# Kernel optimization log

Hardware: AMD Instinct MI355X
Metric: run time of the kernel (lower is better)

## Reference

```python
import jax, jax.numpy as jnp
import numpy as np

B, C, H, W = 32, 1, 28, 896
WW = WS = 28
S = (W - WW) // WS + 1  # 32 windows
CONV_DIM, FC_DIM, NUM_CLASSES = 64, 128, 83
FC_IN = CONV_DIM * (H // 2) * (WW // 2)  # 64*14*14 = 12544


def setup_inputs() -> dict:
    key = jax.random.key(0)
    ks = jax.random.split(key, 9)
    sc = 0.05
    return {
        "x": jax.random.normal(ks[0], (B, C, H, W), jnp.float32),
        "conv1_w": jax.random.normal(ks[1], (CONV_DIM, C, 3, 3), jnp.float32) * sc,
        "conv1_b": jax.random.normal(ks[2], (CONV_DIM,), jnp.float32) * sc,
        "conv2_w": jax.random.normal(ks[3], (CONV_DIM, CONV_DIM, 3, 3), jnp.float32) * sc,
        "conv2_b": jax.random.normal(ks[4], (CONV_DIM,), jnp.float32) * sc,
        "fc1_w": jax.random.normal(ks[5], (FC_DIM, FC_IN), jnp.float32) * sc,
        "fc1_b": jax.random.normal(ks[6], (FC_DIM,), jnp.float32) * sc,
        "fc2_w": jax.random.normal(ks[7], (NUM_CLASSES, FC_DIM), jnp.float32) * sc,
        "fc2_b": jax.random.normal(ks[8], (NUM_CLASSES,), jnp.float32) * sc,
    }


def _conv_relu(x, w, b):
    # 3x3 conv, stride 1, padding 1 (torch Conv2d padding=1), then ReLU
    y = jax.lax.conv_general_dilated(
        x, w, window_strides=(1, 1), padding=((1, 1), (1, 1)),
        dimension_numbers=("NCHW", "OIHW", "NCHW"))
    return jax.nn.relu(y + b[None, :, None, None])


def reference(x, conv1_w, conv1_b, conv2_w, conv2_b, fc1_w, fc1_b, fc2_w, fc2_b):
    Bx = x.shape[0]
    # WS == WW -> non-overlapping windows; extract all S windows at once via reshape
    # (B, C, H, S*WW) -> (B*S, C, H, WW)
    win = x.reshape(Bx, C, H, S, WW).transpose(0, 3, 1, 2, 4).reshape(Bx * S, C, H, WW)
    h = _conv_relu(win, conv1_w, conv1_b)
    h = _conv_relu(h, conv2_w, conv2_b)
    # MaxPool2d(2)
    h = jax.lax.reduce_window(h, -jnp.inf, jax.lax.max,
                              window_dimensions=(1, 1, 2, 2),
                              window_strides=(1, 1, 2, 2), padding="VALID")
    # dropout is identity in eval mode
    h = h.reshape(Bx * S, FC_IN)  # torch.flatten(x, 1) on NCHW matches row-major reshape
    h = jax.nn.relu(h @ fc1_w.T + fc1_b)
    logits = h @ fc2_w.T + fc2_b  # (B*S, num_classes)
    # -> (B, num_classes, S) as in the torch module
    return logits.reshape(Bx, S, NUM_CLASSES).transpose(0, 2, 1)
```

## Files before the change

### kernel.cpp

```cpp
#include <hip/hip_runtime.h>
#include <hip/hip_bf16.h>


typedef __attribute__((ext_vector_type(8))) short short8;
typedef __attribute__((ext_vector_type(4))) float f32x4;

#define WB1_E   0u
#define WB2_E   2048u
#define WFC1_E  38912u
#define WFC2_E  1644544u
#define POOL_E  1656832u
#define PART_B  29003776u

__device__ __forceinline__ unsigned short f2bf(float f) {
  unsigned u = __float_as_uint(f);
  u += 0x7fffu + ((u >> 16) & 1u);
  return (unsigned short)(u >> 16);
}

__global__ __launch_bounds__(256) void prep_kernel(
    const float* __restrict__ w1, const float* __restrict__ c1b,
    const float* __restrict__ w2, const float* __restrict__ wfc1,
    const float* __restrict__ wfc2, unsigned short* __restrict__ ws16)
{
  int i = blockIdx.x * blockDim.x + threadIdx.x;
  if (i < 2048) {
    int j = i & 7, l = (i >> 3) & 63, nt = i >> 9;
    int n = nt * 16 + (l & 15), k = 8 * (l >> 4) + j;
    float v = (k < 9) ? w1[n * 9 + k] : (k == 9 ? c1b[n] : 0.f);
    ws16[WB1_E + i] = f2bf(v);
  } else if (i < 38912) {
    int i2 = i - 2048;
    int j = i2 & 7, l = (i2 >> 3) & 63, rest = i2 >> 9;
    int ks = rest % 18, nt = rest / 18;
    int n = nt * 16 + (l & 15);
    int kk = ks * 32 + 8 * (l >> 4) + j;
    int dydx = kk >> 6, ci = kk & 63;
    ws16[WB2_E + i2] = f2bf(w2[n * 576 + ci * 9 + dydx]);
  } else if (i < 1644544) {
    int i2 = i - 38912;
    int j = i2 & 7, l = (i2 >> 3) & 63, rest = i2 >> 9;
    int ks = rest % 392, nt = rest / 392;
    int fcn = nt * 16 + (l & 15);
    int kp = ks * 32 + 8 * (l >> 4) + j;
    int co = kp & 63, r2 = kp >> 6;
    int oxp = r2 % 14, oyp = r2 / 14;
    ws16[WFC1_E + i2] = f2bf(wfc1[fcn * 12544 + co * 196 + oyp * 14 + oxp]);
  } else if (i < 1656832) {
    int i2 = i - 1644544;
    int j = i2 & 7, l = (i2 >> 3) & 63, rest = i2 >> 9;
    int ks = rest & 3, nt = rest >> 2;
    int cls = nt * 16 + (l & 15);
    int k = ks * 32 + 8 * (l >> 4) + j;
    float v = (cls < 83) ? wfc2[cls * 128 + k] : 0.f;
    ws16[WFC2_E + i2] = f2bf(v);
  }
}

__global__ __launch_bounds__(512, 4) void conv_kernel(
    const float* __restrict__ x, const float* __restrict__ c2b,
    unsigned short* __restrict__ ws16)
{
  extern __shared__ char smem[];
  unsigned short* xw = (unsigned short*)(smem + 69120);

  const int tid = threadIdx.x;
  const int wave = tid >> 6, lane = tid & 63;
  const int g = lane >> 4, l15 = lane & 15;
  const int bid = blockIdx.x;
  const int n = bid >> 1, hf = bid & 1;
  const int r0 = hf ? 16 : 0;
  const int rlo = hf ? 15 : 0;
  const int M1 = hf ? 364 : 476;
  const int T1 = hf ? 23 : 30;
  const int T2 = hf ? 21 : 28;

  const short8* wb1 = (const short8*)(ws16 + WB1_E);
  const short8* wb2 = (const short8*)(ws16 + WB2_E);
  unsigned short* poolg = ws16 + POOL_E + (unsigned)n * 12544u;

  short8 z8 = {0, 0, 0, 0, 0, 0, 0, 0};
  short8* l8 = (short8*)smem;
  for (int idx = tid; idx < 4320; idx += 512) l8[idx] = z8;
  {
    const float* xg = x + (n >> 5) * 25088 + (n & 31) * 28;
    for (int i = tid; i < 784; i += 512)
      xw[i] = f2bf(xg[(i / 28) * 896 + (i % 28)]);
  }
  __syncthreads();

  {
    short8 b1f[4];
#pragma unroll
    for (int nt = 0; nt < 4; ++nt) b1f[nt] = wb1[nt * 64 + lane];
    for (int mt = wave; mt < T1; mt += 8) {
      int m = mt * 16 + l15;
      bool mval = m < M1;
      int mc = mval ? m : M1 - 1;
      int rr = rlo + mc / 28, ox = mc % 28;
      short8 a;
#pragma unroll
      for (int j = 0; j < 8; ++j) {
        int k = 8 * g + j;
        int dy = (k >= 6) ? 2 : ((k >= 3) ? 1 : 0);
        int dx = k - 3 * dy;
        int iy = rr + dy - 1, ix = ox + dx - 1;
        bool valid = (k < 9) && mval && iy >= 0 && iy < 28 && ix >= 0 && ix < 28;
        int idx = valid ? iy * 28 + ix : 0;
        unsigned short v = xw[idx];
        short r = valid ? (short)v : (short)0;
        a[j] = (k == 9) ? (short)0x3F80 : r;
      }
      f32x4 d[4];
#pragma unroll
      for (int nt = 0; nt < 4; ++nt) {
        f32x4 zz = {0.f, 0.f, 0.f, 0.f};
        d[nt] = __builtin_amdgcn_mfma_f32_16x16x32_bf16(b1f[nt], a, zz, 0, 0, 0);
      }
      if (mval) {
        int lr = rr - r0 + 1;
        int sp = lr * 30 + ox + 1;
        unsigned base = (unsigned)sp * 128u;
        unsigned swz = ((unsigned)sp & 7u) << 4;
#pragma unroll
        for (int nt = 0; nt < 4; ++nt)
#pragma unroll
          for (int t = 0; t < 2; ++t) {
            int co2 = nt * 16 + 4 * g + 2 * t;
            unsigned pk = (unsigned)f2bf(fmaxf(d[nt][2 * t], 0.f)) |
                          ((unsigned)f2bf(fmaxf(d[nt][2 * t + 1], 0.f)) << 16);
            *(unsigned*)(smem + (base + (((unsigned)(co2 * 2)) ^ swz))) = pk;
          }
      }
    }
  }
  __syncthreads();

  {
    const int ntp = (wave < 4) ? 0 : 2;
    const int mg = wave & 3;
    float c2bv[2];
#pragma unroll
    for (int tn = 0; tn < 2; ++tn) c2bv[tn] = c2b[(ntp + tn) * 16 + l15];
    const int w4 = l15 >> 2;
    const int oyw = 2 * (w4 >> 1) + ((l15 >> 1) & 1);
    const int oxw = 2 * (w4 & 1) + (l15 & 1);
    int spb[7];
#pragma unroll
    for (int mi = 0; mi < 7; ++mi) {
      int mt = mg + 4 * mi;
      int ryy = (mt * 37) >> 8;
      int rx = mt - 7 * ryy;
      spb[mi] = (4 * ryy + oyw) * 30 + 4 * rx + oxw;
    }
    f32x4 acc[7][2];
#pragma unroll
    for (int mi = 0; mi < 7; ++mi) {
      f32x4 zz = {0.f, 0.f, 0.f, 0.f};
      acc[mi][0] = zz; acc[mi][1] = zz;
    }
#pragma unroll 1
    for (int phase = 0; phase < 6; ++phase) {
      short8 bfr[2][3];
#pragma unroll
      for (int tn = 0; tn < 2; ++tn)
#pragma unroll
        for (int ks = 0; ks < 3; ++ks)
          bfr[tn][ks] = wb2[((ntp + tn) * 18 + phase * 3 + ks) * 64 + lane];
      int dspv[3], cixv[3];
#pragma unroll
      for (int ks = 0; ks < 3; ++ks) {
        int ksg = phase * 3 + ks;
        int dydx = ksg >> 1;
        int dy = (dydx * 11) >> 5;
        int dx = dydx - 3 * dy;
        dspv[ks] = dy * 30 + dx;
        cixv[ks] = ((ksg & 1) << 6) + 16 * g;
      }
#pragma unroll
      for (int mi = 0; mi < 7; ++mi) {
        int mt = mg + 4 * mi;
        if (mt < T2) {
#pragma unroll
          for (int ks = 0; ks < 3; ++ks) {
            int sp = spb[mi] + dspv[ks];
            unsigned off = (unsigned)sp * 128u +
                           (((unsigned)cixv[ks]) ^ ((((unsigned)sp) & 7u) << 4));
            short8 a = *(const short8*)(smem + off);
            acc[mi][0] = __builtin_amdgcn_mfma_f32_16x16x32_bf16(a, bfr[0][ks], acc[mi][0], 0, 0, 0);
            acc[mi][1] = __builtin_amdgcn_mfma_f32_16x16x32_bf16(a, bfr[1][ks], acc[mi][1], 0, 0, 0);
          }
        }
      }
    }
    const int yb = hf ? 8 : 0;
#pragma unroll
    for (int mi = 0; mi < 7; ++mi) {
      int mt = mg + 4 * mi;
      if (mt < T2) {
        int ryy = (mt * 37) >> 8;
        int rx = mt - 7 * ryy;
        int oyp = yb + 2 * ryy + (g >> 1);
        int oxp = 2 * rx + (g & 1);
#pragma unroll
        for (int tn = 0; tn < 2; ++tn) {
          int co = (ntp + tn) * 16 + l15;
          f32x4 v = acc[mi][tn];
          float p = fmaxf(fmaxf(v[0], v[1]), fmaxf(v[2], v[3]));
          p = fmaxf(p + c2bv[tn], 0.f);
          poolg[(oyp * 14 + oxp) * 64 + co] = f2bf(p);
        }
      }
    }
  }
}

__global__ __launch_bounds__(512) void fc1_kernel(unsigned short* __restrict__ ws16)
{
  extern __shared__ char smem[];
  short8* A8 = (short8*)smem;
  const int tid = threadIdx.x;
  const int wave = tid >> 6, lane = tid & 63;
  const int g = lane >> 4, l15 = lane & 15;
  const int ig = blockIdx.x >> 2, q = blockIdx.x & 3;
  const short8* pool8 = (const short8*)(ws16 + POOL_E);
  const short8* wf1 = (const short8*)(ws16 + WFC1_E);
  {
    int img = tid >> 5, l32 = tid & 31;
    const short8* src = pool8 + (ig * 16 + img) * 1568 + q * 392;
#pragma unroll
    for (int j = 0; j < 13; ++j) {
      int idx = l32 + 32 * j;
      if (idx < 392) A8[img * 393 + idx] = src[idx];
    }
  }
  __syncthreads();
  f32x4 acc = {0.f, 0.f, 0.f, 0.f};
  const short8* wbase = wf1 + (wave * 392 + q * 98) * 64 + lane;
#pragma unroll 2
  for (int ks = 0; ks < 98; ++ks) {
    short8 b = wbase[ks * 64];
    short8 a = A8[l15 * 393 + ks * 4 + g];
    acc = __builtin_amdgcn_mfma_f32_16x16x32_bf16(a, b, acc, 0, 0, 0);
  }
  _Float16* part = (_Float16*)((char*)ws16 + PART_B);
  int base = ((q * 64 + ig) * 16 + 4 * g) * 128 + wave * 16 + l15;
#pragma unroll
  for (int i = 0; i < 4; ++i) part[base + i * 128] = (_Float16)acc[i];
}

__global__ __launch_bounds__(512) void fc2_kernel(
    const float* __restrict__ b1, const float* __restrict__ b2,
    const unsigned short* __restrict__ ws16, float* __restrict__ out)
{
  __shared__ unsigned short h_s[16 * 136];
  const int tid = threadIdx.x;
  const int wave = tid >> 6, lane = tid & 63;
  const int g = lane >> 4, l15 = lane & 15;
  const int ig = blockIdx.x;
  const _Float16* part = (const _Float16*)((const char*)ws16 + PART_B);
#pragma unroll
  for (int t = 0; t < 4; ++t) {
    int u = tid + 512 * t;
    int img = u >> 7, fcn = u & 127;
    float s = 0.f;
#pragma unroll
    for (int q2 = 0; q2 < 4; ++q2)
      s += (float)part[((q2 * 64 + ig) * 16 + img) * 128 + fcn];
    h_s[img * 136 + fcn] = f2bf(fmaxf(s + b1[fcn], 0.f));
  }
  __syncthreads();
  if (wave < 6) {
    const short8* wf2 = (const short8*)(ws16 + WFC2_E);
    const short8* h8 = (const short8*)h_s;
    f32x4 a2 = {0.f, 0.f, 0.f, 0.f};
#pragma unroll
    for (int ks = 0; ks < 4; ++ks) {
      short8 b = wf2[(wave * 4 + ks) * 64 + lane];
      short8 a = h8[l15 * 17 + ks * 4 + g];
      a2 = __builtin_amdgcn_mfma_f32_16x16x32_bf16(a, b, a2, 0, 0, 0);
    }
    int cls = wave * 16 + l15;
    if (cls < 83) {
      float bias2 = b2[cls];
#pragma unroll
      for (int i = 0; i < 4; ++i) {
        int nimg = ig * 16 + 4 * g + i;
        out[((nimg >> 5) * 83 + cls) * 32 + (nimg & 31)] = a2[i] + bias2;
      }
    }
  }
}

extern "C" void kernel_launch(void* const* d_in, const int* in_sizes, int n_in,
                              void* d_out, int out_size, void* d_ws, size_t ws_size,
                              hipStream_t stream)
{
  const float* x    = (const float*)d_in[0];
  const float* w1   = (const float*)d_in[1];
  const float* c1b  = (const float*)d_in[2];
  const float* w2   = (const float*)d_in[3];
  const float* c2b  = (const float*)d_in[4];
  const float* wfc1 = (const float*)d_in[5];
  const float* bfc1 = (const float*)d_in[6];
  const float* wfc2 = (const float*)d_in[7];
  const float* bfc2 = (const float*)d_in[8];
  unsigned short* ws16 = (unsigned short*)d_ws;
  float* out = (float*)d_out;

  prep_kernel<<<6472, 256, 0, stream>>>(w1, c1b, w2, wfc1, wfc2, ws16);
  conv_kernel<<<2048, 512, 70688, stream>>>(x, c2b, ws16);
  fc1_kernel<<<256, 512, 100608, stream>>>(ws16);
  fc2_kernel<<<64, 512, 0, stream>>>(bfc1, bfc2, ws16, out);
}
```

Measured before the change: 110.2 us.

## Pad conv LDS layout instead of XOR swizzle and pre-pad input tile

Replaces the XOR-swizzled 128-byte-per-pixel LDS layout for conv1 output with a padded 144-byte stride, so conv2 A-operand addresses become base plus a constant offset. Stores the input window zero-padded to 30x30 in LDS, which lets conv1 im2col gathers drop the per-element bounds checks and divisions. Only lane groups 0 and 1 load real taps. The cost is more LDS per block (about 79.6 KB versus 70.7 KB), which can lower the number of resident blocks per CU.

After: 98.23 us. 1.12x faster.

```diff
diff --git a/kernel.cpp b/kernel.cpp
--- a/kernel.cpp
+++ b/kernel.cpp
@@ -62,30 +62,36 @@
     unsigned short* __restrict__ ws16)
 {
   extern __shared__ char smem[];
-  unsigned short* xw = (unsigned short*)(smem + 69120);
+  unsigned short* xw = (unsigned short*)(smem + 77760);
 
   const int tid = threadIdx.x;
   const int wave = tid >> 6, lane = tid & 63;
   const int g = lane >> 4, l15 = lane & 15;
   const int bid = blockIdx.x;
   const int n = bid >> 1, hf = bid & 1;
-  const int r0 = hf ? 16 : 0;
   const int rlo = hf ? 15 : 0;
   const int M1 = hf ? 364 : 476;
   const int T1 = hf ? 23 : 30;
   const int T2 = hf ? 21 : 28;
+  const int lr_off = hf ? -15 : 1;
 
   const short8* wb1 = (const short8*)(ws16 + WB1_E);
   const short8* wb2 = (const short8*)(ws16 + WB2_E);
   unsigned short* poolg = ws16 + POOL_E + (unsigned)n * 12544u;
 
   short8 z8 = {0, 0, 0, 0, 0, 0, 0, 0};
-  short8* l8 = (short8*)smem;
-  for (int idx = tid; idx < 4320; idx += 512) l8[idx] = z8;
   {
+    short8* l8 = (short8*)smem;
+    for (int idx = tid; idx < 4860; idx += 512) l8[idx] = z8;
     const float* xg = x + (n >> 5) * 25088 + (n & 31) * 28;
-    for (int i = tid; i < 784; i += 512)
-      xw[i] = f2bf(xg[(i / 28) * 896 + (i % 28)]);
+    for (int i = tid; i < 900; i += 512) {
+      int yy = (i * 2185) >> 16;
+      int xx = i - yy * 30;
+      int iy = yy - 1, ix = xx - 1;
+      bool inb = (iy >= 0) && (iy < 28) && (ix >= 0) && (ix < 28);
+      float v = inb ? xg[iy * 896 + ix] : 0.f;
+      xw[i] = f2bf(v);
+    }
   }
   __syncthreads();
 
@@ -97,19 +103,23 @@
       int m = mt * 16 + l15;
       bool mval = m < M1;
       int mc = mval ? m : M1 - 1;
-      int rr = rlo + mc / 28, ox = mc % 28;
-      short8 a;
-#pragma unroll
-      for (int j = 0; j < 8; ++j) {
-        int k = 8 * g + j;
-        int dy = (k >= 6) ? 2 : ((k >= 3) ? 1 : 0);
-        int dx = k - 3 * dy;
-        int iy = rr + dy - 1, ix = ox + dx - 1;
-        bool valid = (k < 9) && mval && iy >= 0 && iy < 28 && ix >= 0 && ix < 28;
-        int idx = valid ? iy * 28 + ix : 0;
-        unsigned short v = xw[idx];
-        short r = valid ? (short)v : (short)0;
-        a[j] = (k == 9) ? (short)0x3F80 : r;
+      int yr = (mc * 2341) >> 16;
+      int rr = rlo + yr;
+      int ox = mc - yr * 28;
+      const char* xb = (const char*)xw + (rr * 30 + ox) * 2;
+      short8 a = z8;
+      if (g == 0) {
+        a[0] = *(const short*)(xb + 0);
+        a[1] = *(const short*)(xb + 2);
+        a[2] = *(const short*)(xb + 4);
+        a[3] = *(const short*)(xb + 60);
+        a[4] = *(const short*)(xb + 62);
+        a[5] = *(const short*)(xb + 64);
+        a[6] = *(const short*)(xb + 120);
+        a[7] = *(const short*)(xb + 122);
+      } else if (g == 1) {
+        a[0] = *(const short*)(xb + 124);
+        a[1] = (short)0x3F80;
       }
       f32x4 d[4];
 #pragma unroll
@@ -118,10 +128,7 @@
         d[nt] = __builtin_amdgcn_mfma_f32_16x16x32_bf16(b1f[nt], a, zz, 0, 0, 0);
       }
       if (mval) {
-        int lr = rr - r0 + 1;
-        int sp = lr * 30 + ox + 1;
-        unsigned base = (unsigned)sp * 128u;
-        unsigned swz = ((unsigned)sp & 7u) << 4;
+        int spB = ((rr + lr_off) * 30 + ox + 1) * 144;
 #pragma unroll
         for (int nt = 0; nt < 4; ++nt)
 #pragma unroll
@@ -129,7 +136,7 @@
             int co2 = nt * 16 + 4 * g + 2 * t;
             unsigned pk = (unsigned)f2bf(fmaxf(d[nt][2 * t], 0.f)) |
                           ((unsigned)f2bf(fmaxf(d[nt][2 * t + 1], 0.f)) << 16);
-            *(unsigned*)(smem + (base + (((unsigned)(co2 * 2)) ^ swz))) = pk;
+            *(unsigned*)(smem + (spB + co2 * 2)) = pk;
           }
       }
     }
@@ -145,13 +152,13 @@
     const int w4 = l15 >> 2;
     const int oyw = 2 * (w4 >> 1) + ((l15 >> 1) & 1);
     const int oxw = 2 * (w4 & 1) + (l15 & 1);
-    int spb[7];
+    int baseB[7];
 #pragma unroll
     for (int mi = 0; mi < 7; ++mi) {
       int mt = mg + 4 * mi;
       int ryy = (mt * 37) >> 8;
       int rx = mt - 7 * ryy;
-      spb[mi] = (4 * ryy + oyw) * 30 + 4 * rx + oxw;
+      baseB[mi] = ((4 * ryy + oyw) * 30 + 4 * rx + oxw) * 144 + 16 * g;
     }
     f32x4 acc[7][2];
 #pragma unroll
@@ -167,15 +174,14 @@
 #pragma unroll
         for (int ks = 0; ks < 3; ++ks)
           bfr[tn][ks] = wb2[((ntp + tn) * 18 + phase * 3 + ks) * 64 + lane];
-      int dspv[3], cixv[3];
+      int dspB[3];
 #pragma unroll
       for (int ks = 0; ks < 3; ++ks) {
         int ksg = phase * 3 + ks;
         int dydx = ksg >> 1;
         int dy = (dydx * 11) >> 5;
         int dx = dydx - 3 * dy;
-        dspv[ks] = dy * 30 + dx;
-        cixv[ks] = ((ksg & 1) << 6) + 16 * g;
+        dspB[ks] = (dy * 30 + dx) * 144 + ((ksg & 1) << 6);
       }
 #pragma unroll
       for (int mi = 0; mi < 7; ++mi) {
@@ -183,10 +189,7 @@
         if (mt < T2) {
 #pragma unroll
           for (int ks = 0; ks < 3; ++ks) {
-            int sp = spb[mi] + dspv[ks];
-            unsigned off = (unsigned)sp * 128u +
-                           (((unsigned)cixv[ks]) ^ ((((unsigned)sp) & 7u) << 4));
-            short8 a = *(const short8*)(smem + off);
+            short8 a = *(const short8*)(smem + (baseB[mi] + dspB[ks]));
             acc[mi][0] = __builtin_amdgcn_mfma_f32_16x16x32_bf16(a, bfr[0][ks], acc[mi][0], 0, 0, 0);
             acc[mi][1] = __builtin_amdgcn_mfma_f32_16x16x32_bf16(a, bfr[1][ks], acc[mi][1], 0, 0, 0);
           }
@@ -309,7 +312,7 @@
   float* out = (float*)d_out;
 
   prep_kernel<<<6472, 256, 0, stream>>>(w1, c1b, w2, wfc1, wfc2, ws16);
-  conv_kernel<<<2048, 512, 70688, stream>>>(x, c2b, ws16);
+  conv_kernel<<<2048, 512, 79616, stream>>>(x, c2b, ws16);
   fc1_kernel<<<256, 512, 100608, stream>>>(ws16);
   fc2_kernel<<<64, 512, 0, stream>>>(bfc1, bfc2, ws16, out);
 }
```
